# Optimization experiments

Measured on AMD Instinct MI355X. Metric: run time of the kernel, lower is better.

The kernel has to match this reference:

```python
import jax, jax.numpy as jnp
import numpy as np
import math

D_MODEL = 1024
NUM_HEADS = 16
B, S = 2, 2048


def setup_inputs() -> dict:
    key = jax.random.key(0)
    ks = jax.random.split(key, 11)
    def w(k):
        return jax.random.normal(k, (D_MODEL, D_MODEL), dtype=jnp.float32) * 0.02
    def b(k):
        return jax.random.normal(k, (D_MODEL,), dtype=jnp.float32) * 0.02
    # causal mask, broadcastable to [B, H, S, S]
    mask = jnp.tril(jnp.ones((S, S), dtype=jnp.int32))[None, None, :, :]
    return {
        "q": jax.random.normal(ks[0], (B, S, D_MODEL), dtype=jnp.float32),
        "k": jax.random.normal(ks[1], (B, S, D_MODEL), dtype=jnp.float32),
        "v": jax.random.normal(ks[2], (B, S, D_MODEL), dtype=jnp.float32),
        "mask": mask,
        "w_q": w(ks[3]), "b_q": b(ks[4]),
        "w_k": w(ks[5]), "b_k": b(ks[6]),
        "w_v": w(ks[7]), "b_v": b(ks[8]),
        "w_o": w(ks[9]), "b_o": b(ks[10]),
    }


def reference(q, k, v, mask, w_q, b_q, w_k, b_k, w_v, b_v, w_o, b_o):
    B_, S_, D = q.shape
    H = NUM_HEADS
    dk = D // H
    # torch Linear: x @ W^T + b; then split heads -> [B, H, S, dk]
    def proj(x, W, b):
        return (x @ W.T + b).reshape(B_, S_, H, dk).transpose(0, 2, 1, 3)
    Q = proj(q, w_q, b_q)
    K = proj(k, w_k, b_k)
    V = proj(v, w_v, b_v)
    scores = jnp.einsum('bhqd,bhkd->bhqk', Q, K) / math.sqrt(dk)
    scores = jnp.where(mask == 0, jnp.float32(-1e9), scores)
    attn = jax.nn.softmax(scores, axis=-1)  # dropout p=0.0 -> identity
    x = jnp.einsum('bhqk,bhkd->bhqd', attn, V)
    x = x.transpose(0, 2, 1, 3).reshape(B_, S_, D)
    return x @ w_o.T + b_o
```

## Files before the change

kernel.cpp:

```cpp
#include <hip/hip_runtime.h>
#include <stdint.h>

#define BATCH 2
#define SEQ   2048
#define DM    1024
#define NH    16
#define DK    64

#define MEG4 4194304UL
#define MEG1 1048576UL
#define STAGE_BASE (4 * MEG4)
#define SB         (8 * MEG4)

#define QSCALE 0.18033688011112042f

typedef __bf16 v8bf __attribute__((ext_vector_type(8)));
typedef float  v4f  __attribute__((ext_vector_type(4)));

#define GLDS(g, l) __builtin_amdgcn_global_load_lds(                          \
    (const __attribute__((address_space(1))) uint32_t*)(g),                   \
    (__attribute__((address_space(3))) uint32_t*)(l), 16, 0, 0)

static __device__ __forceinline__ float bf2f(uint16_t u) {
    union { uint32_t i; float f; } c; c.i = ((uint32_t)u) << 16; return c.f;
}
static __device__ __forceinline__ uint16_t f2bf(float f) {
    union { float f; uint32_t i; } c; c.f = f;
    uint32_t x = c.i;
    return (uint16_t)((x + 0x7fffu + ((x >> 16) & 1u)) >> 16);
}
static __device__ __forceinline__ uint32_t f2bf_pk(float a, float b) {
#if __has_builtin(__builtin_amdgcn_cvt_pk_bf16_f32)
    typedef __bf16 v2bf __attribute__((ext_vector_type(2)));
    union { v2bf v; uint32_t u; } c;
    c.v = __builtin_amdgcn_cvt_pk_bf16_f32(a, b);
    return c.u;
#else
    union { float f; uint32_t i; } ca, cb; ca.f = a; cb.f = b;
    return (ca.i >> 16) | (cb.i & 0xFFFF0000u);
#endif
}
static __device__ __forceinline__ float fast_exp2(float x) {
#if __has_builtin(__builtin_amdgcn_exp2f)
    return __builtin_amdgcn_exp2f(x);
#else
    return __exp2f(x);
#endif
}

__global__ __launch_bounds__(256) void convert_kernel(
    const float* s0, const float* s1, const float* s2, const float* s3,
    const float* s4, const float* s5, const float* s6, const float* s7,
    const float* s8, const float* s9, const float* s10,
    uint16_t* __restrict__ ws)
{
    constexpr size_t SZ[11]  = {MEG4, MEG4, MEG4, MEG1, 1024, MEG1, 1024,
                                MEG1, 1024, MEG1, 1024};
    constexpr size_t OFF[11] = {STAGE_BASE, STAGE_BASE + MEG4, STAGE_BASE + 2 * MEG4,
                                7 * MEG4,          SB + 0,
                                7 * MEG4 + MEG1,   SB + 1024,
                                7 * MEG4 + 2*MEG1, SB + 2048,
                                7 * MEG4 + 3*MEG1, SB + 3072};
    const int z = blockIdx.y;
    size_t i0 = ((size_t)blockIdx.x * 256 + threadIdx.x) * 8;
    if (i0 >= SZ[z]) return;
    const float* src;
    switch (z) {
        case 0: src = s0; break;  case 1: src = s1; break;
        case 2: src = s2; break;  case 3: src = s3; break;
        case 4: src = s4; break;  case 5: src = s5; break;
        case 6: src = s6; break;  case 7: src = s7; break;
        case 8: src = s8; break;  case 9: src = s9; break;
        default: src = s10; break;
    }
    const float* s = src + i0;
    uint16_t* dst = ws + OFF[z] + i0;
#pragma unroll
    for (int t = 0; t < 8; t++) dst[t] = f2bf(s[t]);
}

__device__ __forceinline__ void gemm_core(const uint16_t* __restrict__ A,
                                          const uint16_t* __restrict__ W,
                                          const uint16_t* __restrict__ bias,
                                          void* __restrict__ C,
                                          int m0, int n0, int mode, float scale)
{
    constexpr int N = DM, K = DM;
    __shared__ __align__(16) uint16_t sA[64][64];
    __shared__ __align__(16) uint16_t sB[128][64];

    const int tid  = threadIdx.x;
    const int lane = tid & 63;
    const int wid  = tid >> 6;
    const int ln15 = lane & 15;
    const int quad = lane >> 4;

    v4f acc[4][2];
    const v4f vzero = {0.f, 0.f, 0.f, 0.f};
#pragma unroll
    for (int i = 0; i < 4; i++)
#pragma unroll
        for (int j = 0; j < 2; j++) acc[i][j] = vzero;

    const int srow = lane >> 3;
    const int schk = lane & 7;
    const int scol = (schk ^ srow) * 8;
    const int key = ln15 & 7;

    for (int k0 = 0; k0 < K; k0 += 64) {
#pragma unroll
        for (int c = 0; c < 2; c++) {
            int rA = wid * 16 + c * 8;
            GLDS(&A[(size_t)(m0 + rA + srow) * K + k0 + scol], &sA[rA][0]);
        }
#pragma unroll
        for (int c = 0; c < 4; c++) {
            int rB = wid * 32 + c * 8;
            GLDS(&W[(size_t)(n0 + rB + srow) * K + k0 + scol], &sB[rB][0]);
        }
        __syncthreads();

#pragma unroll
        for (int s = 0; s < 2; s++) {
            v8bf af[4], bfv[2];
#pragma unroll
            for (int i = 0; i < 4; i++) {
                int pc = (s * 4 + quad) ^ key;
                af[i] = *(const v8bf*)&sA[i * 16 + ln15][pc * 8];
            }
#pragma unroll
            for (int j = 0; j < 2; j++) {
                int pc = (s * 4 + quad) ^ key;
                bfv[j] = *(const v8bf*)&sB[wid * 32 + j * 16 + ln15][pc * 8];
            }
#pragma unroll
            for (int i = 0; i < 4; i++)
#pragma unroll
                for (int j = 0; j < 2; j++)
                    acc[i][j] = __builtin_amdgcn_mfma_f32_16x16x32_bf16(
                        af[i], bfv[j], acc[i][j], 0, 0, 0);
        }
        __syncthreads();
    }

#pragma unroll
    for (int i = 0; i < 4; i++) {
#pragma unroll
        for (int j = 0; j < 2; j++) {
#pragma unroll
            for (int r = 0; r < 4; r++) {
                int m = m0 + i * 16 + quad * 4 + r;
                int n = n0 + wid * 32 + j * 16 + ln15;
                float val = (acc[i][j][r] + bf2f(bias[n])) * scale;
                if (mode == 3) {
                    ((float*)C)[(size_t)m * N + n] = val;
                } else {
                    int b = m >> 11, s = m & (SEQ - 1);
                    int h = n >> 6,  d = n & (DK - 1);
                    size_t idx;
                    if (mode == 2)
                        idx = (((size_t)(b * NH + h) * DK + d) * SEQ) + s;
                    else
                        idx = (((size_t)(b * NH + h) * SEQ + s) * DK) + d;
                    ((uint16_t*)C)[idx] = f2bf(val);
                }
            }
        }
    }
}

__global__ __launch_bounds__(256) void qkv_proj_kernel(
    const uint16_t* __restrict__ qa_, const uint16_t* __restrict__ ka_,
    const uint16_t* __restrict__ va_,
    const uint16_t* __restrict__ wq, const uint16_t* __restrict__ bq,
    const uint16_t* __restrict__ wk, const uint16_t* __restrict__ bk,
    const uint16_t* __restrict__ wv, const uint16_t* __restrict__ bv,
    uint16_t* __restrict__ qo, uint16_t* __restrict__ ko,
    uint16_t* __restrict__ vto)
{
    const int seg = blockIdx.y >> 3;
    const int n0  = (blockIdx.y & 7) * 128;
    const int m0  = blockIdx.x * 64;
    const uint16_t* A  = (seg == 0) ? qa_ : (seg == 1) ? ka_ : va_;
    const uint16_t* W  = (seg == 0) ? wq : (seg == 1) ? wk : wv;
    const uint16_t* Bi = (seg == 0) ? bq : (seg == 1) ? bk : bv;
    uint16_t*       O  = (seg == 0) ? qo : (seg == 1) ? ko : vto;
    gemm_core(A, W, Bi, O, m0, n0, (seg == 2) ? 2 : 0,
              (seg == 0) ? QSCALE : 1.0f);
}

__global__ __launch_bounds__(256) void out_proj_kernel(
    const uint16_t* __restrict__ A, const uint16_t* __restrict__ W,
    const uint16_t* __restrict__ Bi, float* __restrict__ O)
{
    gemm_core(A, W, Bi, O, blockIdx.x * 64, blockIdx.y * 128, 3, 1.0f);
}

__global__ __launch_bounds__(256) void attn_kernel(
    const uint16_t* __restrict__ Qw, const uint16_t* __restrict__ Kw,
    const uint16_t* __restrict__ VTw, uint16_t* __restrict__ Ow)
{
    __shared__ __align__(16) uint16_t sK[128][72];
    __shared__ __align__(16) uint16_t sVT[64][136];
    __shared__ __align__(16) uint16_t sP[128][136];

    const int tid  = threadIdx.x;
    const int lane = tid & 63;
    const int wid  = tid >> 6;
    const int ln15 = lane & 15;
    const int quad = lane >> 4;
    const int h = blockIdx.x, p = blockIdx.y, b = blockIdx.z;
    const float NEG = -30000.0f;

    const int qt[2]   = { p, 31 - p };
    const int jmax[2] = { p >> 1, (31 - p) >> 1 };

    const uint16_t* Qb  = Qw  + (size_t)(b * NH + h) * SEQ * DK;
    const uint16_t* Kb  = Kw  + (size_t)(b * NH + h) * SEQ * DK;
    const uint16_t* VTb = VTw + (size_t)(b * NH + h) * DK * SEQ;

    v8bf qa[2][2];
#pragma unroll
    for (int t = 0; t < 2; t++)
#pragma unroll
        for (int ks = 0; ks < 2; ks++)
            qa[t][ks] = *(const v8bf*)&Qb[(size_t)(qt[t] * 64 + wid * 16 + ln15) * DK
                                          + ks * 32 + quad * 8];

    const v4f vzero = {0.f, 0.f, 0.f, 0.f};
    v4f o_acc[2][4];
#pragma unroll
    for (int t = 0; t < 2; t++)
#pragma unroll
        for (int tn = 0; tn < 4; tn++) o_acc[t][tn] = vzero;
    float lrow[2][4];
#pragma unroll
    for (int t = 0; t < 2; t++)
#pragma unroll
        for (int r = 0; r < 4; r++) lrow[t][r] = 0.f;

    for (int j = 0; j <= jmax[1]; j++) {
        __syncthreads();

        const uint16_t* Ksrc = Kb + (size_t)j * 128 * DK;
#pragma unroll
        for (int t4 = 0; t4 < 4; t4++) {
            int s = tid + t4 * 256;
            int row = s >> 3, cs = (s & 7) * 8;
            *(uint4*)&sK[row][cs] = *(const uint4*)&Ksrc[(size_t)row * DK + cs];
        }
#pragma unroll
        for (int t4 = 0; t4 < 4; t4++) {
            int s = tid + t4 * 256;
            int row = s >> 4, cs = (s & 15) * 8;
            *(uint4*)&sVT[row][cs] =
                *(const uint4*)&VTb[(size_t)row * SEQ + j * 128 + cs];
        }
        __syncthreads();

#pragma unroll
        for (int t = 0; t < 2; t++) {
            if (j > jmax[t]) continue;
            v4f sacc[8];
#pragma unroll
            for (int tn = 0; tn < 8; tn++) sacc[tn] = vzero;
#pragma unroll
            for (int tn = 0; tn < 8; tn++) {
                v8bf k0 = *(const v8bf*)&sK[tn * 16 + ln15][quad * 8];
                v8bf k1 = *(const v8bf*)&sK[tn * 16 + ln15][32 + quad * 8];
                sacc[tn] = __builtin_amdgcn_mfma_f32_16x16x32_bf16(
                    qa[t][0], k0, sacc[tn], 0, 0, 0);
                sacc[tn] = __builtin_amdgcn_mfma_f32_16x16x32_bf16(
                    qa[t][1], k1, sacc[tn], 0, 0, 0);
            }
            const bool diag = (j == (qt[t] >> 1));
#pragma unroll
            for (int r = 0; r < 4; r++) {
                int rloc = quad * 4 + r;
                int grow = qt[t] * 64 + wid * 16 + rloc;
                float pe[8];
                float rs = 0.f;
#pragma unroll
                for (int tn = 0; tn < 8; tn++) {
                    float x = sacc[tn][r];
                    if (diag) {
                        int col = j * 128 + tn * 16 + ln15;
                        if (col > grow) x = NEG;
                    }
                    float pv = fast_exp2(x);
                    pe[tn] = pv;
                    rs += pv;
                }
                uint16_t* prow = &sP[t * 64 + wid * 16 + rloc][ln15];
#pragma unroll
                for (int tp = 0; tp < 4; tp++) {
                    uint32_t pk2 = f2bf_pk(pe[2 * tp], pe[2 * tp + 1]);
                    prow[(2 * tp) * 16]     = (uint16_t)pk2;
                    prow[(2 * tp + 1) * 16] = (uint16_t)(pk2 >> 16);
                }
                lrow[t][r] += rs;
            }
        }

#pragma unroll
        for (int t = 0; t < 2; t++) {
            if (j > jmax[t]) continue;
#pragma unroll
            for (int ks = 0; ks < 4; ks++) {
                v8bf pf = *(const v8bf*)&sP[t * 64 + wid * 16 + ln15][ks * 32 + quad * 8];
#pragma unroll
                for (int tn4 = 0; tn4 < 4; tn4++) {
                    v8bf vf = *(const v8bf*)&sVT[tn4 * 16 + ln15][ks * 32 + quad * 8];
                    o_acc[t][tn4] = __builtin_amdgcn_mfma_f32_16x16x32_bf16(
                        pf, vf, o_acc[t][tn4], 0, 0, 0);
                }
            }
        }
    }

#pragma unroll
    for (int t = 0; t < 2; t++)
#pragma unroll
        for (int r = 0; r < 4; r++)
#pragma unroll
            for (int off = 1; off < 16; off <<= 1)
                lrow[t][r] += __shfl_xor(lrow[t][r], off, 64);

#pragma unroll
    for (int t = 0; t < 2; t++) {
#pragma unroll
        for (int r = 0; r < 4; r++) {
            float inv = 1.f / fmaxf(lrow[t][r], 1e-20f);
            int grow = qt[t] * 64 + wid * 16 + quad * 4 + r;
#pragma unroll
            for (int tn4 = 0; tn4 < 4; tn4++) {
                int d = tn4 * 16 + ln15;
                float val = o_acc[t][tn4][r] * inv;
                Ow[((size_t)b * SEQ + grow) * DM + h * DK + d] = f2bf(val);
            }
        }
    }
}

extern "C" void kernel_launch(void* const* d_in, const int* in_sizes, int n_in,
                              void* d_out, int out_size, void* d_ws, size_t ws_size,
                              hipStream_t stream)
{
    (void)in_sizes; (void)n_in; (void)out_size; (void)ws_size;
    uint16_t* ws = (uint16_t*)d_ws;

    uint16_t* q_ws  = ws;
    uint16_t* k_ws  = ws + MEG4;
    uint16_t* vt_ws = ws + 2 * MEG4;
    uint16_t* o_ws  = ws + 3 * MEG4;
    uint16_t* qs  = ws + STAGE_BASE;
    uint16_t* ks  = ws + STAGE_BASE + MEG4;
    uint16_t* vs  = ws + STAGE_BASE + 2 * MEG4;
    uint16_t* wqs = ws + 7 * MEG4;
    uint16_t* wks = ws + 7 * MEG4 + MEG1;
    uint16_t* wvs = ws + 7 * MEG4 + 2 * MEG1;
    uint16_t* wos = ws + 7 * MEG4 + 3 * MEG1;
    uint16_t* bqs = ws + SB;
    uint16_t* bks = ws + SB + 1024;
    uint16_t* bvs = ws + SB + 2048;
    uint16_t* bos = ws + SB + 3072;

    convert_kernel<<<dim3(2048, 11), 256, 0, stream>>>(
        (const float*)d_in[0], (const float*)d_in[1], (const float*)d_in[2],
        (const float*)d_in[4], (const float*)d_in[5], (const float*)d_in[6],
        (const float*)d_in[7], (const float*)d_in[8], (const float*)d_in[9],
        (const float*)d_in[10], (const float*)d_in[11], ws);

    dim3 blk(256);
    qkv_proj_kernel<<<dim3(64, 24), blk, 0, stream>>>(
        qs, ks, vs, wqs, bqs, wks, bks, wvs, bvs, q_ws, k_ws, vt_ws);
    attn_kernel<<<dim3(NH, 16, BATCH), blk, 0, stream>>>(
        q_ws, k_ws, vt_ws, o_ws);
    out_proj_kernel<<<dim3(64, 8), blk, 0, stream>>>(o_ws, wos, bos, (float*)d_out);
}
```

Baseline: 229.7 us.

## Register-prefetch next K/V tile in attention loop and raise occupancy hint

The attention kernel now loads the next K and V^T tiles from global memory into registers right after the shared-memory store and barrier. Those loads are in flight while the current tile's MFMA and softmax work runs, which is meant to hide global load latency behind compute. It also adds a min-blocks-per-CU hint of 2 to launch_bounds. The prefetch buffers add 32 VGPRs, and together with the occupancy hint this may increase register pressure or cause spills.

```diff
diff --git a/kernel.cpp b/kernel.cpp
--- a/kernel.cpp
+++ b/kernel.cpp
@@ -196,7 +196,7 @@
     gemm_core(A, W, Bi, O, blockIdx.x * 64, blockIdx.y * 128, 3, 1.0f);
 }
 
-__global__ __launch_bounds__(256) void attn_kernel(
+__global__ __launch_bounds__(256, 2) void attn_kernel(
     const uint16_t* __restrict__ Qw, const uint16_t* __restrict__ Kw,
     const uint16_t* __restrict__ VTw, uint16_t* __restrict__ Ow)
 {
@@ -239,24 +239,34 @@
 #pragma unroll
         for (int r = 0; r < 4; r++) lrow[t][r] = 0.f;
 
+    uint4 pk[4], pv[4];
+    const int krow = tid >> 3, kcol = (tid & 7) * 8;
+    const int vrow = tid >> 4, vcol = (tid & 15) * 8;
+#pragma unroll
+    for (int t4 = 0; t4 < 4; t4++) {
+        pk[t4] = *(const uint4*)&Kb[(size_t)(krow + t4 * 32) * DK + kcol];
+        pv[t4] = *(const uint4*)&VTb[(size_t)(vrow + t4 * 16) * SEQ + vcol];
+    }
+
     for (int j = 0; j <= jmax[1]; j++) {
         __syncthreads();
 
-        const uint16_t* Ksrc = Kb + (size_t)j * 128 * DK;
 #pragma unroll
         for (int t4 = 0; t4 < 4; t4++) {
-            int s = tid + t4 * 256;
-            int row = s >> 3, cs = (s & 7) * 8;
-            *(uint4*)&sK[row][cs] = *(const uint4*)&Ksrc[(size_t)row * DK + cs];
-        }
-#pragma unroll
-        for (int t4 = 0; t4 < 4; t4++) {
-            int s = tid + t4 * 256;
-            int row = s >> 4, cs = (s & 15) * 8;
-            *(uint4*)&sVT[row][cs] =
-                *(const uint4*)&VTb[(size_t)row * SEQ + j * 128 + cs];
+            *(uint4*)&sK[krow + t4 * 32][kcol]  = pk[t4];
+            *(uint4*)&sVT[vrow + t4 * 16][vcol] = pv[t4];
         }
         __syncthreads();
+
+        if (j < jmax[1]) {
+            const uint16_t* Ksrc = Kb + (size_t)(j + 1) * 128 * DK;
+            const uint16_t* Vsrc = VTb + (size_t)(j + 1) * 128;
+#pragma unroll
+            for (int t4 = 0; t4 < 4; t4++) {
+                pk[t4] = *(const uint4*)&Ksrc[(size_t)(krow + t4 * 32) * DK + kcol];
+                pv[t4] = *(const uint4*)&Vsrc[(size_t)(vrow + t4 * 16) * SEQ + vcol];
+            }
+        }
 
 #pragma unroll
         for (int t = 0; t < 2; t++) {
@@ -287,9 +297,9 @@
                         int col = j * 128 + tn * 16 + ln15;
                         if (col > grow) x = NEG;
                     }
-                    float pv = fast_exp2(x);
-                    pe[tn] = pv;
-                    rs += pv;
+                    float pvv = fast_exp2(x);
+                    pe[tn] = pvv;
+                    rs += pvv;
                 }
                 uint16_t* prow = &sP[t * 64 + wid * 16 + rloc][ln15];
 #pragma unroll
```

Result: slower. 272.4 us (+18.6%).

## Compute transposed scores so P stays in registers for PV MFMA

Applied to the files above, without the earlier changes.

The attention kernel now computes S^T = K·Q^T, which puts each query row's scores in the lane layout that a 16x16x16 bf16 MFMA expects as its B operand. P is packed straight into registers and multiplied as O^T = V^T·P^T, so the shared-memory P buffer and its scattered 16-bit stores and reads are gone. Row sums shrink to one accumulator per lane with two cross-quad shuffles. In exchange it issues twice as many smaller K=16 MFMAs for the PV product, reads V^T with 8-byte LDS loads, and writes the output with a strided scatter.

```diff
diff --git a/kernel.cpp b/kernel.cpp
--- a/kernel.cpp
+++ b/kernel.cpp
@@ -16,6 +16,7 @@
 
 typedef __bf16 v8bf __attribute__((ext_vector_type(8)));
 typedef float  v4f  __attribute__((ext_vector_type(4)));
+typedef short  v4s  __attribute__((ext_vector_type(4)));
 
 #define GLDS(g, l) __builtin_amdgcn_global_load_lds(                          \
     (const __attribute__((address_space(1))) uint32_t*)(g),                   \
@@ -45,6 +46,15 @@
     return __builtin_amdgcn_exp2f(x);
 #else
     return __exp2f(x);
+#endif
+}
+static __device__ __forceinline__ v4f mfma16_bf16(v4s a, v4s b, v4f c) {
+#if __has_builtin(__builtin_amdgcn_mfma_f32_16x16x16_bf16)
+    typedef __bf16 v4bf __attribute__((ext_vector_type(4)));
+    union { v4s s; v4bf v; } ua, ub; ua.s = a; ub.s = b;
+    return __builtin_amdgcn_mfma_f32_16x16x16_bf16(ua.v, ub.v, c, 0, 0, 0);
+#else
+    return __builtin_amdgcn_mfma_f32_16x16x16bf16_1k(a, b, c, 0, 0, 0);
 #endif
 }
 
@@ -202,7 +212,6 @@
 {
     __shared__ __align__(16) uint16_t sK[128][72];
     __shared__ __align__(16) uint16_t sVT[64][136];
-    __shared__ __align__(16) uint16_t sP[128][136];
 
     const int tid  = threadIdx.x;
     const int lane = tid & 63;
@@ -219,25 +228,21 @@
     const uint16_t* Kb  = Kw  + (size_t)(b * NH + h) * SEQ * DK;
     const uint16_t* VTb = VTw + (size_t)(b * NH + h) * DK * SEQ;
 
-    v8bf qa[2][2];
+    v8bf qb[2][2];
 #pragma unroll
     for (int t = 0; t < 2; t++)
 #pragma unroll
         for (int ks = 0; ks < 2; ks++)
-            qa[t][ks] = *(const v8bf*)&Qb[(size_t)(qt[t] * 64 + wid * 16 + ln15) * DK
+            qb[t][ks] = *(const v8bf*)&Qb[(size_t)(qt[t] * 64 + wid * 16 + ln15) * DK
                                           + ks * 32 + quad * 8];
 
     const v4f vzero = {0.f, 0.f, 0.f, 0.f};
-    v4f o_acc[2][4];
+    v4f oT[2][4];
 #pragma unroll
     for (int t = 0; t < 2; t++)
 #pragma unroll
-        for (int tn = 0; tn < 4; tn++) o_acc[t][tn] = vzero;
-    float lrow[2][4];
-#pragma unroll
-    for (int t = 0; t < 2; t++)
-#pragma unroll
-        for (int r = 0; r < 4; r++) lrow[t][r] = 0.f;
+        for (int dm = 0; dm < 4; dm++) oT[t][dm] = vzero;
+    float lrow[2] = {0.f, 0.f};
 
     for (int j = 0; j <= jmax[1]; j++) {
         __syncthreads();
@@ -261,82 +266,73 @@
 #pragma unroll
         for (int t = 0; t < 2; t++) {
             if (j > jmax[t]) continue;
-            v4f sacc[8];
-#pragma unroll
-            for (int tn = 0; tn < 8; tn++) sacc[tn] = vzero;
+
+            v4f st[8];
+#pragma unroll
+            for (int tn = 0; tn < 8; tn++) st[tn] = vzero;
 #pragma unroll
             for (int tn = 0; tn < 8; tn++) {
                 v8bf k0 = *(const v8bf*)&sK[tn * 16 + ln15][quad * 8];
                 v8bf k1 = *(const v8bf*)&sK[tn * 16 + ln15][32 + quad * 8];
-                sacc[tn] = __builtin_amdgcn_mfma_f32_16x16x32_bf16(
-                    qa[t][0], k0, sacc[tn], 0, 0, 0);
-                sacc[tn] = __builtin_amdgcn_mfma_f32_16x16x32_bf16(
-                    qa[t][1], k1, sacc[tn], 0, 0, 0);
-            }
+                st[tn] = __builtin_amdgcn_mfma_f32_16x16x32_bf16(
+                    k0, qb[t][0], st[tn], 0, 0, 0);
+                st[tn] = __builtin_amdgcn_mfma_f32_16x16x32_bf16(
+                    k1, qb[t][1], st[tn], 0, 0, 0);
+            }
+
             const bool diag = (j == (qt[t] >> 1));
+            const int qrow = qt[t] * 64 + wid * 16 + ln15;
+            v4s pfrag[8];
+#pragma unroll
+            for (int tn = 0; tn < 8; tn++) {
+                float pe[4];
+#pragma unroll
+                for (int r = 0; r < 4; r++) {
+                    float x = st[tn][r];
+                    if (diag) {
+                        int keyg = j * 128 + tn * 16 + quad * 4 + r;
+                        if (keyg > qrow) x = NEG;
+                    }
+                    pe[r] = fast_exp2(x);
+                    lrow[t] += pe[r];
+                }
+                union { uint32_t u[2]; v4s s; } c;
+                c.u[0] = f2bf_pk(pe[0], pe[1]);
+                c.u[1] = f2bf_pk(pe[2], pe[3]);
+                pfrag[tn] = c.s;
+            }
+
+#pragma unroll
+            for (int dm = 0; dm < 4; dm++) {
+#pragma unroll
+                for (int tn = 0; tn < 8; tn++) {
+                    union { uint32_t u[2]; v4s s; } va;
+                    const uint32_t* vp = (const uint32_t*)
+                        &sVT[dm * 16 + ln15][tn * 16 + quad * 4];
+                    va.u[0] = vp[0]; va.u[1] = vp[1];
+                    oT[t][dm] = mfma16_bf16(va.s, pfrag[tn], oT[t][dm]);
+                }
+            }
+        }
+    }
+
+#pragma unroll
+    for (int t = 0; t < 2; t++) {
+        lrow[t] += __shfl_xor(lrow[t], 16, 64);
+        lrow[t] += __shfl_xor(lrow[t], 32, 64);
+    }
+
+#pragma unroll
+    for (int t = 0; t < 2; t++) {
+        float inv = 1.f / fmaxf(lrow[t], 1e-20f);
+        int grow = qt[t] * 64 + wid * 16 + ln15;
+#pragma unroll
+        for (int dm = 0; dm < 4; dm++) {
 #pragma unroll
             for (int r = 0; r < 4; r++) {
-                int rloc = quad * 4 + r;
-                int grow = qt[t] * 64 + wid * 16 + rloc;
-                float pe[8];
-                float rs = 0.f;
-#pragma unroll
-                for (int tn = 0; tn < 8; tn++) {
-                    float x = sacc[tn][r];
-                    if (diag) {
-                        int col = j * 128 + tn * 16 + ln15;
-                        if (col > grow) x = NEG;
-                    }
-                    float pv = fast_exp2(x);
-                    pe[tn] = pv;
-                    rs += pv;
-                }
-                uint16_t* prow = &sP[t * 64 + wid * 16 + rloc][ln15];
-#pragma unroll
-                for (int tp = 0; tp < 4; tp++) {
-                    uint32_t pk2 = f2bf_pk(pe[2 * tp], pe[2 * tp + 1]);
-                    prow[(2 * tp) * 16]     = (uint16_t)pk2;
-                    prow[(2 * tp + 1) * 16] = (uint16_t)(pk2 >> 16);
-                }
-                lrow[t][r] += rs;
-            }
-        }
-
-#pragma unroll
-        for (int t = 0; t < 2; t++) {
-            if (j > jmax[t]) continue;
-#pragma unroll
-            for (int ks = 0; ks < 4; ks++) {
-                v8bf pf = *(const v8bf*)&sP[t * 64 + wid * 16 + ln15][ks * 32 + quad * 8];
-#pragma unroll
-                for (int tn4 = 0; tn4 < 4; tn4++) {
-                    v8bf vf = *(const v8bf*)&sVT[tn4 * 16 + ln15][ks * 32 + quad * 8];
-                    o_acc[t][tn4] = __builtin_amdgcn_mfma_f32_16x16x32_bf16(
-                        pf, vf, o_acc[t][tn4], 0, 0, 0);
-                }
-            }
-        }
-    }
-
-#pragma unroll
-    for (int t = 0; t < 2; t++)
-#pragma unroll
-        for (int r = 0; r < 4; r++)
-#pragma unroll
-            for (int off = 1; off < 16; off <<= 1)
-                lrow[t][r] += __shfl_xor(lrow[t][r], off, 64);
-
-#pragma unroll
-    for (int t = 0; t < 2; t++) {
-#pragma unroll
-        for (int r = 0; r < 4; r++) {
-            float inv = 1.f / fmaxf(lrow[t][r], 1e-20f);
-            int grow = qt[t] * 64 + wid * 16 + quad * 4 + r;
-#pragma unroll
-            for (int tn4 = 0; tn4 < 4; tn4++) {
-                int d = tn4 * 16 + ln15;
-                float val = o_acc[t][tn4][r] * inv;
-                Ow[((size_t)b * SEQ + grow) * DM + h * DK + d] = f2bf(val);
+                int d = dm * 16 + quad * 4 + r;
+                Ow[((size_t)b * SEQ + grow) * DM + h * DK + d] =
+                    f2bf(oT[t][dm][r] * inv);
             }
         }
     }
```

Measured after the change: 227.8 us. About the same (-0.8%).
